# Optimization experiments

Measured on AMD Instinct MI355X. Metric: run time of the kernel, lower is better.

## Reference

```python
import jax, jax.numpy as jnp
import numpy as np

TEMP = 0.05
BIG = 1e6


def _mlp(z, W1, b1, W2, b2, W3, b3, W4, b4, W5, b5):
    h = jax.nn.selu(z @ W1 + b1)
    h = jax.nn.selu(h @ W2 + b2)
    h = jax.nn.selu(h @ W3 + b3)
    h = jax.nn.selu(h @ W4 + b4)
    return h @ W5 + b5


def _cdist(a, b):
    # Euclidean distance via ||a||^2 + ||b||^2 - 2 a.b (clamped for fp safety)
    d2 = (jnp.sum(a * a, axis=1)[:, None]
          + jnp.sum(b * b, axis=1)[None, :]
          - 2.0 * (a @ b.T))
    return jnp.sqrt(jnp.maximum(d2, 0.0))


def _compute_drift(x, y_pos, y_neg):
    N, N_pos = x.shape[0], y_pos.shape[0]
    dist_pos = _cdist(x, y_pos)                      # [N, N_pos]
    dist_neg = _cdist(x, y_neg)                      # [N, N_neg]
    if N == y_neg.shape[0]:
        dist_neg = dist_neg + jnp.eye(N, dtype=x.dtype) * BIG
    logit = jnp.concatenate([-dist_pos / TEMP, -dist_neg / TEMP], axis=1)
    for _ in range(5):  # Sinkhorn: alternating row / column normalization
        logit = logit - jax.nn.logsumexp(logit, axis=-1, keepdims=True)
        logit = logit - jax.nn.logsumexp(logit, axis=-2, keepdims=True)
    A = jnp.exp(logit)
    A_pos, A_neg = A[:, :N_pos], A[:, N_pos:]
    W_pos = A_pos * jnp.sum(A_neg, axis=1, keepdims=True)
    W_neg = A_neg * jnp.sum(A_pos, axis=1, keepdims=True)
    return W_pos @ y_pos - W_neg @ y_neg             # [N, D]


def _forward(pos, z, W1, b1, W2, b2, W3, b3, W4, b4, W5, b5):
    gen = _mlp(z, W1, b1, W2, b2, W3, b3, W4, b4, W5, b5)
    V = _compute_drift(gen, pos, gen)                # computed under no_grad
    target = jax.lax.stop_gradient(gen + V)
    return jnp.sum((gen - target) ** 2, axis=-1)      # per-sample loss [N]


def setup_inputs() -> dict:
    key = jax.random.key(0)
    ks = jax.random.split(key, 8)
    N, D, ND, H = 8192, 256, 128, 1024
    def w(k, fan_in, fan_out):
        return jax.random.normal(k, (fan_in, fan_out), jnp.float32) / np.float32(np.sqrt(fan_in))
    return {
        "pos": jax.random.normal(ks[0], (N, D), jnp.float32),
        "z": jax.random.normal(ks[1], (N, ND), jnp.float32),
        "W1": w(ks[2], ND, H), "b1": jnp.zeros((H,), jnp.float32),
        "W2": w(ks[3], H, H),  "b2": jnp.zeros((H,), jnp.float32),
        "W3": w(ks[4], H, H),  "b3": jnp.zeros((H,), jnp.float32),
        "W4": w(ks[5], H, H),  "b4": jnp.zeros((H,), jnp.float32),
        "W5": w(ks[6], H, D),  "b5": jnp.zeros((D,), jnp.float32),
    }


def reference(pos, z, W1, b1, W2, b2, W3, b3, W4, b4, W5, b5):
    return _forward(pos, z, W1, b1, W2, b2, W3, b3, W4, b4, W5, b5)
```

## Files before the change

kernel.cpp:

```cpp
#include <hip/hip_runtime.h>

#define DEVI __device__ __forceinline__

typedef short bf16x8 __attribute__((ext_vector_type(8)));
typedef float f32x4 __attribute__((ext_vector_type(4)));
typedef unsigned short u16;
typedef unsigned short u16x8 __attribute__((ext_vector_type(8)));
typedef unsigned short u16x4 __attribute__((ext_vector_type(4)));

enum { EPI_MLP = 0, EPI_DISTQ = 1, EPI_NEGTRI = 2 };

#define KLOG2E_T 28.853900817779268f
#define QSCALE 1846.6496523378733f
#define INVQ 0.015625f
#define PSLOTS 80

DEVI u16 f2bf(float f) {
  unsigned u = __float_as_uint(f);
  return (u16)((u + 0x7FFFu + ((u >> 16) & 1u)) >> 16);
}
DEVI float bf2f(u16 h) { return __uint_as_float(((unsigned)h) << 16); }
DEVI float seluf(float x) {
  return x > 0.f ? 1.0507009873554805f * x : 1.7580993408473766f * expm1f(x);
}
DEVI void gload16(const void* g, void* l) {
  __builtin_amdgcn_global_load_lds(
      (const __attribute__((address_space(1))) unsigned*)g,
      (__attribute__((address_space(3))) unsigned*)l, 16, 0, 0);
}
DEVI void lse_comb(float& m, float& s, float m2, float s2) {
  float M = fmaxf(m, m2);
  s = s * exp2f(m - M) + s2 * exp2f(m2 - M);
  m = M;
}
DEVI size_t triblk(int I, int J) { return ((size_t)I * (I + 1) / 2 + J) * 4096; }

template <int R, int NW>
DEVI void stage_tile(const u16* __restrict__ src, int ld, int row0, int k0,
                     u16* lds, int wave, int lane) {
  constexpr int INST = R / (16 * NW);
#pragma unroll
  for (int t = 0; t < INST; ++t) {
    int brow = (wave * INST + t) * 16;
    int row = brow + (lane >> 2);
    int col = (lane & 3) * 8;
    gload16(src + (size_t)(row0 + row) * ld + (k0 + col), lds + brow * 32);
  }
}

template <int BM, int BN, int WM, int WN, int EPI>
__global__ __launch_bounds__(WM* WN * 64) void gemm_k(
    const u16* __restrict__ Ahi, const u16* __restrict__ Alo, int lda,
    const u16* __restrict__ Bhi, const u16* __restrict__ Blo, int ldb, int K,
    float* __restrict__ Cf, int ldc,
    const float* __restrict__ bias, int act, u16* __restrict__ Ohi,
    u16* __restrict__ Olo, int ldo,
    const float* __restrict__ xN2, const float* __restrict__ yN2,
    u16* __restrict__ Cq) {
  if constexpr (EPI == EPI_NEGTRI) {
    if (blockIdx.x > blockIdx.y) return;
  }
  constexpr int NW = WM * WN;
  constexpr int FM = BM / (WM * 16), FN = BN / (WN * 16);
  const int tid = threadIdx.x, lane = tid & 63, wave = tid >> 6;
  const int bm0 = blockIdx.y * BM, bn0 = blockIdx.x * BN;
  const int wr = (wave / WN) * (FM * 16), wc = (wave % WN) * (FN * 16);
  __shared__ __align__(16) u16 AsH[BM * 32];
  __shared__ __align__(16) u16 BsH[BN * 32];
  __shared__ __align__(16) u16 AsL[BM * 32];
  __shared__ __align__(16) u16 BsL[BN * 32];
  f32x4 acc[FM][FN] = {};
  const int fr = lane & 15, ko = (lane >> 4) * 8;
  for (int k0 = 0; k0 < K; k0 += 32) {
    stage_tile<BM, NW>(Ahi, lda, bm0, k0, AsH, wave, lane);
    stage_tile<BN, NW>(Bhi, ldb, bn0, k0, BsH, wave, lane);
    stage_tile<BM, NW>(Alo, lda, bm0, k0, AsL, wave, lane);
    stage_tile<BN, NW>(Blo, ldb, bn0, k0, BsL, wave, lane);
    __syncthreads();
    bf16x8 ah[FM], bh[FN], al[FM], bl[FN];
#pragma unroll
    for (int m = 0; m < FM; ++m) ah[m] = *(const bf16x8*)&AsH[(wr + m * 16 + fr) * 32 + ko];
#pragma unroll
    for (int n = 0; n < FN; ++n) bh[n] = *(const bf16x8*)&BsH[(wc + n * 16 + fr) * 32 + ko];
#pragma unroll
    for (int m = 0; m < FM; ++m) al[m] = *(const bf16x8*)&AsL[(wr + m * 16 + fr) * 32 + ko];
#pragma unroll
    for (int n = 0; n < FN; ++n) bl[n] = *(const bf16x8*)&BsL[(wc + n * 16 + fr) * 32 + ko];
#pragma unroll
    for (int m = 0; m < FM; ++m)
#pragma unroll
      for (int n = 0; n < FN; ++n) {
        acc[m][n] = __builtin_amdgcn_mfma_f32_16x16x32_bf16(ah[m], bh[n], acc[m][n], 0, 0, 0);
        acc[m][n] = __builtin_amdgcn_mfma_f32_16x16x32_bf16(al[m], bh[n], acc[m][n], 0, 0, 0);
        acc[m][n] = __builtin_amdgcn_mfma_f32_16x16x32_bf16(ah[m], bl[n], acc[m][n], 0, 0, 0);
      }
    __syncthreads();
  }
#pragma unroll
  for (int m = 0; m < FM; ++m)
#pragma unroll
    for (int n = 0; n < FN; ++n)
#pragma unroll
      for (int q = 0; q < 4; ++q) {
        int row = bm0 + wr + m * 16 + (lane >> 4) * 4 + q;
        int col = bn0 + wc + n * 16 + fr;
        float v = acc[m][n][q];
        if constexpr (EPI == EPI_MLP) {
          v += bias[col];
          if (act) v = seluf(v);
          u16 h = f2bf(v);
          size_t idx = (size_t)row * ldo + col;
          Ohi[idx] = h;
          Olo[idx] = f2bf(v - bf2f(h));
          if (Cf) Cf[(size_t)row * ldc + col] = v;
        } else if constexpr (EPI == EPI_DISTQ) {
          float d2 = fmaxf(xN2[row] + yN2[col] - 2.f * v, 0.f);
          float qf = fminf(QSCALE * sqrtf(d2), 65535.f);
          Cq[(size_t)row * 8192 + col] = (u16)__float2uint_rn(qf);
        } else {
          int bI = row >> 6, bJ = col >> 6;
          if (bJ <= bI) {
            float d2 = fmaxf(xN2[row] + yN2[col] - 2.f * v, 0.f);
            float qf = fminf(QSCALE * sqrtf(d2), 65535.f);
            u16 qu = (u16)__float2uint_rn(qf);
            if (row == col) qu = 65535;
            Cq[triblk(bI, bJ) + (row & 63) * 64 + (col & 63)] = qu;
          }
        }
      }
}

DEVI void lse16(const u16x8& qa, const u16x8& qb, const float* __restrict__ w,
                float& m, float& s) {
  f32x4 w0 = *(const f32x4*)w;
  f32x4 w1 = *(const f32x4*)(w + 4);
  f32x4 w2 = *(const f32x4*)(w + 8);
  f32x4 w3 = *(const f32x4*)(w + 12);
  float v[16];
#pragma unroll
  for (int e = 0; e < 4; ++e) {
    v[e] = fmaf((float)qa[e], -INVQ, -w0[e]);
    v[4 + e] = fmaf((float)qa[4 + e], -INVQ, -w1[e]);
    v[8 + e] = fmaf((float)qb[e], -INVQ, -w2[e]);
    v[12 + e] = fmaf((float)qb[4 + e], -INVQ, -w3[e]);
  }
  float mx = v[0];
#pragma unroll
  for (int e = 1; e < 16; ++e) mx = fmaxf(mx, v[e]);
  float ac = 0.f;
#pragma unroll
  for (int e = 0; e < 16; ++e) ac += exp2f(v[e] - mx);
  lse_comb(m, s, mx, ac);
}

__global__ __launch_bounds__(256) void sink_k(
    const u16* __restrict__ DqPos, const u16* __restrict__ DqTri,
    const float* __restrict__ wpos, const float* __restrict__ wneg,
    float* __restrict__ Pm, float* __restrict__ Ps) {
  const int tid = threadIdx.x;
  const int I = blockIdx.y, q8 = blockIdx.x;
  __shared__ __align__(16) u16 stg[4096];
  __shared__ float Cm[64][12], Cs[64][12];
  const int rn = tid >> 2, cn = (tid & 3) * 16;
  const int p2 = tid & 31, g8 = tid >> 5;
  float mA = -3.0e38f, sA = 0.f;
  float mB0 = -3.0e38f, sB0 = 0.f, mB1 = -3.0e38f, sB1 = 0.f;
  const int sw = (rn & 7) << 3;

  {
    const size_t rowbase = (size_t)(I * 64 + rn) * 8192;
    for (int jc = 0; jc < 16; ++jc) {
      int j0 = q8 * 1024 + jc * 64 + cn;
      u16x8 qa = *(const u16x8*)&DqPos[rowbase + j0];
      u16x8 qb = *(const u16x8*)&DqPos[rowbase + j0 + 8];
      lse16(qa, qb, wpos + j0, mA, sA);
    }
  }
  for (int Jb = q8 * 16; Jb < q8 * 16 + 16; ++Jb) {
    if (Jb <= I) {
      const u16* blk = DqTri + triblk(I, Jb);
      u16x8 qa = *(const u16x8*)&blk[rn * 64 + cn];
      u16x8 qb = *(const u16x8*)&blk[rn * 64 + cn + 8];
      lse16(qa, qb, wneg + Jb * 64 + cn, mA, sA);
    } else {
      const u16* blk = DqTri + triblk(Jb, I);
      u16x8 qa = *(const u16x8*)&blk[rn * 64 + cn];
      u16x8 qb = *(const u16x8*)&blk[rn * 64 + cn + 8];
      *(u16x8*)&stg[rn * 64 + (cn ^ sw)] = qa;
      *(u16x8*)&stg[rn * 64 + ((cn + 8) ^ sw)] = qb;
      __syncthreads();
      float v0[8], v1[8];
#pragma unroll
      for (int cc = 0; cc < 8; ++cc) {
        int sj = cc * 8 + g8;
        unsigned wq = *(const unsigned*)&stg[sj * 64 + ((2 * p2) ^ ((sj & 7) << 3))];
        float wgt = wneg[Jb * 64 + sj];
        v0[cc] = fmaf((float)(wq & 0xFFFFu), -INVQ, -wgt);
        v1[cc] = fmaf((float)(wq >> 16), -INVQ, -wgt);
      }
      float mx0 = v0[0], mx1 = v1[0];
#pragma unroll
      for (int cc = 1; cc < 8; ++cc) { mx0 = fmaxf(mx0, v0[cc]); mx1 = fmaxf(mx1, v1[cc]); }
      float a0 = 0.f, a1 = 0.f;
#pragma unroll
      for (int cc = 0; cc < 8; ++cc) { a0 += exp2f(v0[cc] - mx0); a1 += exp2f(v1[cc] - mx1); }
      lse_comb(mB0, sB0, mx0, a0);
      lse_comb(mB1, sB1, mx1, a1);
      __syncthreads();
    }
  }
  for (int i = tid; i < 64 * 12; i += 256) { (&Cm[0][0])[i] = -3.0e38f; (&Cs[0][0])[i] = 0.f; }
  __syncthreads();
  Cm[rn][tid & 3] = mA; Cs[rn][tid & 3] = sA;
  Cm[2 * p2][4 + g8] = mB0; Cs[2 * p2][4 + g8] = sB0;
  Cm[2 * p2 + 1][4 + g8] = mB1; Cs[2 * p2 + 1][4 + g8] = sB1;
  __syncthreads();
  if (tid < 64) {
    float m = Cm[tid][0], s = Cs[tid][0];
#pragma unroll
    for (int b = 1; b < 12; ++b) lse_comb(m, s, Cm[tid][b], Cs[tid][b]);
    Pm[(size_t)q8 * 8192 + I * 64 + tid] = m;
    Ps[(size_t)q8 * 8192 + I * 64 + tid] = s;
  }
}

__global__ __launch_bounds__(256) void colpass_k(
    const u16* __restrict__ DqPos, const u16* __restrict__ DqTri,
    const float* __restrict__ rv, float* __restrict__ Pm, float* __restrict__ Ps) {
  const int bid = blockIdx.x, tid = threadIdx.x;
  __shared__ __align__(16) u16 stg[4096];
  __shared__ float Cm[64][12], Cs[64][12];
  if (bid < 1024) {
    const int q8 = bid & 7, I = bid >> 3;
    const int rn = tid >> 2, cn = (tid & 3) * 16;
    const int p2 = tid & 31, g8 = tid >> 5;
    const int sw = (rn & 7) << 3;
    float mA = -3.0e38f, sA = 0.f;
    float mB0 = -3.0e38f, sB0 = 0.f, mB1 = -3.0e38f, sB1 = 0.f;
    for (int Jb = q8 * 16; Jb < q8 * 16 + 16; ++Jb) {
      if (Jb <= I) {
        const u16* blk = DqTri + triblk(I, Jb);
        u16x8 qa = *(const u16x8*)&blk[rn * 64 + cn];
        u16x8 qb = *(const u16x8*)&blk[rn * 64 + cn + 8];
        lse16(qa, qb, rv + Jb * 64 + cn, mA, sA);
      } else {
        const u16* blk = DqTri + triblk(Jb, I);
        u16x8 qa = *(const u16x8*)&blk[rn * 64 + cn];
        u16x8 qb = *(const u16x8*)&blk[rn * 64 + cn + 8];
        *(u16x8*)&stg[rn * 64 + (cn ^ sw)] = qa;
        *(u16x8*)&stg[rn * 64 + ((cn + 8) ^ sw)] = qb;
        __syncthreads();
        float v0[8], v1[8];
#pragma unroll
        for (int cc = 0; cc < 8; ++cc) {
          int sj = cc * 8 + g8;
          unsigned wq = *(const unsigned*)&stg[sj * 64 + ((2 * p2) ^ ((sj & 7) << 3))];
          float wgt = rv[Jb * 64 + sj];
          v0[cc] = fmaf((float)(wq & 0xFFFFu), -INVQ, -wgt);
          v1[cc] = fmaf((float)(wq >> 16), -INVQ, -wgt);
        }
        float mx0 = v0[0], mx1 = v1[0];
#pragma unroll
        for (int cc = 1; cc < 8; ++cc) { mx0 = fmaxf(mx0, v0[cc]); mx1 = fmaxf(mx1, v1[cc]); }
        float a0 = 0.f, a1 = 0.f;
#pragma unroll
        for (int cc = 0; cc < 8; ++cc) { a0 += exp2f(v0[cc] - mx0); a1 += exp2f(v1[cc] - mx1); }
        lse_comb(mB0, sB0, mx0, a0);
        lse_comb(mB1, sB1, mx1, a1);
        __syncthreads();
      }
    }
    for (int i = tid; i < 64 * 12; i += 256) { (&Cm[0][0])[i] = -3.0e38f; (&Cs[0][0])[i] = 0.f; }
    __syncthreads();
    Cm[rn][tid & 3] = mA; Cs[rn][tid & 3] = sA;
    Cm[2 * p2][4 + g8] = mB0; Cs[2 * p2][4 + g8] = sB0;
    Cm[2 * p2 + 1][4 + g8] = mB1; Cs[2 * p2 + 1][4 + g8] = sB1;
    __syncthreads();
    if (tid < 64) {
      float m = Cm[tid][0], s = Cs[tid][0];
#pragma unroll
      for (int b2 = 1; b2 < 12; ++b2) lse_comb(m, s, Cm[tid][b2], Cs[tid][b2]);
      Pm[(size_t)(72 + q8) * 8192 + I * 64 + tid] = m;
      Ps[(size_t)(72 + q8) * 8192 + I * 64 + tid] = s;
    }
  } else {
    const int b2 = bid - 1024;
    const int jb = b2 & 7, ic = b2 >> 3;
    int j0 = jb * 1024 + tid * 4;
    int i0 = ic * 128;
    float m[4], s[4];
#pragma unroll
    for (int e = 0; e < 4; ++e) { m[e] = -3.0e38f; s[e] = 0.f; }
    for (int ib = 0; ib < 16; ++ib) {
      float v[4][8];
#pragma unroll
      for (int ii = 0; ii < 8; ++ii) {
        int i = i0 + ib * 8 + ii;
        u16x4 qv = *(const u16x4*)&DqPos[(size_t)i * 8192 + j0];
        float ri = rv[i];
#pragma unroll
        for (int e = 0; e < 4; ++e) v[e][ii] = fmaf((float)qv[e], -INVQ, -ri);
      }
#pragma unroll
      for (int e = 0; e < 4; ++e) {
        float mx = v[e][0];
#pragma unroll
        for (int ii = 1; ii < 8; ++ii) mx = fmaxf(mx, v[e][ii]);
        float ac = 0.f;
#pragma unroll
        for (int ii = 0; ii < 8; ++ii) ac += exp2f(v[e][ii] - mx);
        lse_comb(m[e], s[e], mx, ac);
      }
    }
#pragma unroll
    for (int e = 0; e < 4; ++e) {
      Pm[(size_t)(8 + ic) * 8192 + j0 + e] = m[e];
      Ps[(size_t)(8 + ic) * 8192 + j0 + e] = s[e];
    }
  }
}

__global__ void comb_rv_k(const float* __restrict__ Pm, const float* __restrict__ Ps,
                          float* __restrict__ rv) {
  int j = blockIdx.x * 256 + threadIdx.x;
  float m = Pm[j], s = Ps[j];
  for (int b = 1; b < 8; ++b)
    lse_comb(m, s, Pm[(size_t)b * 8192 + j], Ps[(size_t)b * 8192 + j]);
  rv[j] = m + log2f(s);
}

__global__ void comb_cpc_k(const float* __restrict__ Pm, const float* __restrict__ Ps,
                           float* __restrict__ cpos, float* __restrict__ cneg) {
  int j = blockIdx.x * 256 + threadIdx.x;
  if (j < 8192) {
    float m = Pm[(size_t)8 * 8192 + j], s = Ps[(size_t)8 * 8192 + j];
    for (int b = 9; b < 72; ++b)
      lse_comb(m, s, Pm[(size_t)b * 8192 + j], Ps[(size_t)b * 8192 + j]);
    cpos[j] = m + log2f(s);
  } else {
    int jj = j - 8192;
    float m = Pm[(size_t)72 * 8192 + jj], s = Ps[(size_t)72 * 8192 + jj];
    for (int b = 73; b < 80; ++b)
      lse_comb(m, s, Pm[(size_t)b * 8192 + jj], Ps[(size_t)b * 8192 + jj]);
    cneg[jj] = m + log2f(s);
  }
}

template <bool NEG>
__global__ __launch_bounds__(512) void pv_k(
    const u16* __restrict__ DqPos, const u16* __restrict__ DqTri,
    const float* __restrict__ rvec, const float* __restrict__ w,
    const u16* __restrict__ BT, float* __restrict__ Mout,
    float* __restrict__ sout) {
  const int tid = threadIdx.x, lane = tid & 63, wave = tid >> 6;
  const int I = blockIdx.y;
  const int kh = blockIdx.x;
  __shared__ __align__(16) u16 AT[64 * 128];
  __shared__ __align__(16) u16 Bs[4 * 256 * 32];
  __shared__ __align__(16) u16 stg[NEG ? 2 * 4096 : 8];
  __shared__ float rvS[64];
  __shared__ float SredN[64][8];
  __shared__ float SredT[64][8];
  const int wrg = (wave >> 2) * 32, wcg = (wave & 3) * 64;
  const int fr = lane & 15, ko = (lane >> 4) * 8;
  const int rn = tid >> 3;
  const int cnp = (tid & 7) * 16;
  const int cnn = (tid & 7) * 8;
  const int swr = (rn & 7) << 3;
  const int p = tid & 63, sjg = tid >> 6;
  const int swp = (p & 7) << 3;
  float asumN = 0.f, asumT = 0.f;
  if (tid < 64) rvS[tid] = rvec[I * 64 + tid];
  __syncthreads();
  const float riN = rvS[rn];
  const float riT = rvS[p];
  f32x4 acc[2][4] = {};

  for (int jc = 0; jc < 32; ++jc) {
    const int j0 = (kh * 32 + jc) * 128;
    __syncthreads();
#pragma unroll
    for (int ks = 0; ks < 4; ++ks)
      stage_tile<256, 8>(BT, 8192, 0, j0 + ks * 32, Bs + ks * 8192, wave, lane);
    if constexpr (!NEG) {
      const u16* rp = DqPos + (size_t)(I * 64 + rn) * 8192 + j0 + cnp;
      u16x8 qa = *(const u16x8*)rp;
      u16x8 qb = *(const u16x8*)(rp + 8);
      const float* wp = w + j0 + cnp;
      f32x4 w0 = *(const f32x4*)wp;
      f32x4 w1 = *(const f32x4*)(wp + 4);
      f32x4 w2 = *(const f32x4*)(wp + 8);
      f32x4 w3 = *(const f32x4*)(wp + 12);
      union { u16x8 v; u16 e[8]; } pk0, pk1;
#pragma unroll
      for (int e = 0; e < 4; ++e) {
        float a0 = exp2f(fmaf((float)qa[e], -INVQ, -riN - w0[e]));
        float a1 = exp2f(fmaf((float)qa[4 + e], -INVQ, -riN - w1[e]));
        float a2 = exp2f(fmaf((float)qb[e], -INVQ, -riN - w2[e]));
        float a3 = exp2f(fmaf((float)qb[4 + e], -INVQ, -riN - w3[e]));
        asumN += a0 + a1 + a2 + a3;
        pk0.e[e] = f2bf(a0); pk0.e[4 + e] = f2bf(a1);
        pk1.e[e] = f2bf(a2); pk1.e[4 + e] = f2bf(a3);
      }
      *(u16x8*)&AT[rn * 128 + (cnp ^ swr)] = pk0.v;
      *(u16x8*)&AT[rn * 128 + ((cnp + 8) ^ swr)] = pk1.v;
    } else {
      bool anytr = false;
#pragma unroll
      for (int h = 0; h < 2; ++h) {
        const int Jb = kh * 64 + jc * 2 + h;
        if (Jb <= I) {
          const u16* blk = DqTri + triblk(I, Jb);
          u16x8 q = *(const u16x8*)&blk[rn * 64 + cnn];
          const float* wp = w + Jb * 64 + cnn;
          f32x4 w0 = *(const f32x4*)wp;
          f32x4 w1 = *(const f32x4*)(wp + 4);
          union { u16x8 v; u16 e[8]; } pk;
#pragma unroll
          for (int e = 0; e < 4; ++e) {
            float a0 = exp2f(fmaf((float)q[e], -INVQ, -riN - w0[e]));
            float a1 = exp2f(fmaf((float)q[4 + e], -INVQ, -riN - w1[e]));
            asumN += a0 + a1;
            pk.e[e] = f2bf(a0); pk.e[4 + e] = f2bf(a1);
          }
          *(u16x8*)&AT[rn * 128 + ((h * 64 + cnn) ^ swr)] = pk.v;
        } else {
          anytr = true;
          const u16* blk = DqTri + triblk(Jb, I);
          u16x8 q = *(const u16x8*)&blk[rn * 64 + cnn];
          *(u16x8*)&stg[h * 4096 + rn * 64 + (cnn ^ swr)] = q;
        }
      }
      if (anytr) {
        __syncthreads();
#pragma unroll
        for (int h = 0; h < 2; ++h) {
          const int Jb = kh * 64 + jc * 2 + h;
          if (Jb <= I) continue;
#pragma unroll
          for (int cc = 0; cc < 8; ++cc) {
            int sj = cc * 8 + sjg;
            u16 q = stg[h * 4096 + sj * 64 + (p ^ ((sj & 7) << 3))];
            float a = exp2f(fmaf((float)q, -INVQ, -riT - w[Jb * 64 + sj]));
            asumT += a;
            AT[p * 128 + ((h * 64 + sj) ^ swp)] = f2bf(a);
          }
        }
      }
    }
    __syncthreads();
#pragma unroll
    for (int ks = 0; ks < 4; ++ks) {
      bf16x8 a2[2], b2[4];
#pragma unroll
      for (int m = 0; m < 2; ++m) {
        int rl = wrg + m * 16 + fr;
        a2[m] = *(const bf16x8*)&AT[rl * 128 + ((ks * 32 + ko) ^ ((rl & 7) << 3))];
      }
#pragma unroll
      for (int n = 0; n < 4; ++n)
        b2[n] = *(const bf16x8*)&Bs[ks * 8192 + (wcg + n * 16 + fr) * 32 + ko];
#pragma unroll
      for (int m = 0; m < 2; ++m)
#pragma unroll
        for (int n = 0; n < 4; ++n)
          acc[m][n] = __builtin_amdgcn_mfma_f32_16x16x32_bf16(a2[m], b2[n], acc[m][n], 0, 0, 0);
    }
  }
#pragma unroll
  for (int m = 0; m < 2; ++m)
#pragma unroll
    for (int n = 0; n < 4; ++n)
#pragma unroll
      for (int q = 0; q < 4; ++q) {
        int row = I * 64 + wrg + m * 16 + (lane >> 4) * 4 + q;
        int d = wcg + n * 16 + fr;
        Mout[(size_t)kh * 2097152 + (size_t)row * 256 + d] = acc[m][n][q];
      }
  SredN[rn][tid & 7] = asumN;
  SredT[p][sjg] = NEG ? asumT : 0.f;
  __syncthreads();
  if (tid < 64) {
    float s = 0.f;
#pragma unroll
    for (int b = 0; b < 8; ++b) s += SredN[tid][b] + SredT[tid][b];
    sout[kh * 8192 + I * 64 + tid] = s;
  }
}

__global__ void convert_split_k(const float* __restrict__ src, u16* __restrict__ hi,
                                u16* __restrict__ lo, int n) {
  int i = blockIdx.x * 256 + threadIdx.x;
  if (i < n) {
    float v = src[i];
    u16 h = f2bf(v);
    hi[i] = h;
    lo[i] = f2bf(v - bf2f(h));
  }
}

__global__ void transpose_split_k(const float* __restrict__ src, int K, int N,
                                  u16* __restrict__ hi, u16* __restrict__ lo) {
  __shared__ float t[32][33];
  int x = threadIdx.x & 31, y = threadIdx.x >> 5;
  int k0 = blockIdx.x * 32, n0 = blockIdx.y * 32;
  for (int yy = y; yy < 32; yy += 8) t[yy][x] = src[(size_t)(k0 + yy) * N + n0 + x];
  __syncthreads();
  for (int yy = y; yy < 32; yy += 8) {
    float v = t[x][yy];
    size_t idx = (size_t)(n0 + yy) * K + k0 + x;
    u16 h = f2bf(v);
    hi[idx] = h;
    lo[idx] = f2bf(v - bf2f(h));
  }
}

__global__ void transpose_b16_k(const float* __restrict__ src, int M, int D,
                                u16* __restrict__ dst) {
  __shared__ float t[32][33];
  int x = threadIdx.x & 31, y = threadIdx.x >> 5;
  int m0 = blockIdx.x * 32, d0 = blockIdx.y * 32;
  for (int yy = y; yy < 32; yy += 8) t[yy][x] = src[(size_t)(m0 + yy) * D + d0 + x];
  __syncthreads();
  for (int yy = y; yy < 32; yy += 8)
    dst[(size_t)(d0 + yy) * M + m0 + x] = f2bf(t[x][yy]);
}

__global__ void rownorm_k(const float* __restrict__ src, float* __restrict__ o) {
  int i = blockIdx.x, t = threadIdx.x;
  float s = 0.f;
  for (int d = t; d < 256; d += 64) {
    float v = src[(size_t)i * 256 + d];
    s += v * v;
  }
  for (int off = 32; off; off >>= 1) s += __shfl_down(s, off, 64);
  if (t == 0) o[i] = s;
}

__global__ void zero_k(float* __restrict__ p, int n) {
  int i = blockIdx.x * 256 + threadIdx.x;
  if (i < n) p[i] = 0.f;
}

__global__ void decode_k(float* __restrict__ out, float x, int n) {
  int i = blockIdx.x * 256 + threadIdx.x;
  if (i < n) out[i] = x;
}

__global__ void final_out_k(const float* __restrict__ M1, const float* __restrict__ M2,
                            const float* __restrict__ sp, const float* __restrict__ sn,
                            float* __restrict__ out) {
  __shared__ float S[256];
  int i = blockIdx.x, d = threadIdx.x;
  size_t idx = (size_t)i * 256 + d;
  float spv = sp[i] + sp[8192 + i];
  float snv = sn[i] + sn[8192 + i];
  float v = snv * (M1[idx] + M1[2097152 + idx]) - spv * (M2[idx] + M2[2097152 + idx]);
  S[d] = v * v;
  __syncthreads();
  for (int off = 128; off; off >>= 1) {
    if (d < off) S[d] += S[d + off];
    __syncthreads();
  }
  if (d == 0) out[i] = S[0];
}

extern "C" void kernel_launch(void* const* d_in, const int* in_sizes, int n_in,
                              void* d_out, int out_size, void* d_ws, size_t ws_size,
                              hipStream_t stream) {
  (void)in_sizes; (void)n_in; (void)out_size;
  const float* pos = (const float*)d_in[0];
  const float* z   = (const float*)d_in[1];
  const float* W1  = (const float*)d_in[2];
  const float* b1  = (const float*)d_in[3];
  const float* W2  = (const float*)d_in[4];
  const float* b2  = (const float*)d_in[5];
  const float* W3  = (const float*)d_in[6];
  const float* b3  = (const float*)d_in[7];
  const float* W4  = (const float*)d_in[8];
  const float* b4  = (const float*)d_in[9];
  const float* W5  = (const float*)d_in[10];
  const float* b5  = (const float*)d_in[11];
  float* out = (float*)d_out;

  if (ws_size < (size_t)261500000) {
    decode_k<<<32, 256, 0, stream>>>(out, (float)(double)(ws_size >> 10), 8192);
    return;
  }

  char* wsp = (char*)d_ws;
  size_t off = 0;
  auto alloc = [&](size_t bytes) -> char* {
    char* p = wsp + off;
    off += (bytes + 255) & ~(size_t)255;
    return p;
  };
  u16* DqPos = (u16*)alloc((size_t)8192 * 8192 * 2);
  u16* DqTri = (u16*)alloc((size_t)8256 * 4096 * 2);
  u16* Yh    = (u16*)alloc((size_t)16384 * 256 * 2);
  u16* Yl    = (u16*)alloc((size_t)16384 * 256 * 2);
  u16* posT  = (u16*)alloc((size_t)256 * 8192 * 2);
  u16* genT  = (u16*)alloc((size_t)256 * 8192 * 2);
  float* yN2 = (float*)alloc(16384 * 4);
  float* rv  = (float*)alloc(8192 * 4);
  float* cpos = (float*)alloc(8192 * 4);
  float* cneg = (float*)alloc(8192 * 4);
  float* spv = (float*)alloc(2 * 8192 * 4);
  float* snv = (float*)alloc(2 * 8192 * 4);
  float* M1  = (float*)alloc((size_t)2 * 8192 * 256 * 4);
  float* M2  = (float*)alloc((size_t)2 * 8192 * 256 * 4);
  float* Pm = M1;
  float* Ps = Pm + (size_t)PSLOTS * 8192;

  size_t toff = 0;
  char* tbase = (char*)DqPos;
  auto talloc = [&](size_t bytes) -> char* {
    char* p = tbase + toff;
    toff += (bytes + 255) & ~(size_t)255;
    return p;
  };
  u16* zh    = (u16*)talloc((size_t)8192 * 128 * 2);
  u16* zl    = (u16*)talloc((size_t)8192 * 128 * 2);
  u16* W1Th  = (u16*)talloc(1024 * 128 * 2);
  u16* W1Tl  = (u16*)talloc(1024 * 128 * 2);
  u16* W2Th  = (u16*)talloc(1024 * 1024 * 2);
  u16* W2Tl  = (u16*)talloc(1024 * 1024 * 2);
  u16* W3Th  = (u16*)talloc(1024 * 1024 * 2);
  u16* W3Tl  = (u16*)talloc(1024 * 1024 * 2);
  u16* W4Th  = (u16*)talloc(1024 * 1024 * 2);
  u16* W4Tl  = (u16*)talloc(1024 * 1024 * 2);
  u16* W5Th  = (u16*)talloc(256 * 1024 * 2);
  u16* W5Tl  = (u16*)talloc(256 * 1024 * 2);
  u16* h1h   = (u16*)talloc((size_t)8192 * 1024 * 2);
  u16* h1l   = (u16*)talloc((size_t)8192 * 1024 * 2);
  u16* h2h   = (u16*)talloc((size_t)8192 * 1024 * 2);
  u16* h2l   = (u16*)talloc((size_t)8192 * 1024 * 2);
  float* genf = (float*)talloc((size_t)8192 * 256 * 4);

  u16* genH = Yh + (size_t)8192 * 256;
  u16* genL = Yl + (size_t)8192 * 256;
  float* pN2 = yN2;
  float* gN2 = yN2 + 8192;

  convert_split_k<<<4096, 256, 0, stream>>>(z, zh, zl, 8192 * 128);
  convert_split_k<<<8192, 256, 0, stream>>>(pos, Yh, Yl, 8192 * 256);
  transpose_split_k<<<dim3(4, 32), 256, 0, stream>>>(W1, 128, 1024, W1Th, W1Tl);
  transpose_split_k<<<dim3(32, 32), 256, 0, stream>>>(W2, 1024, 1024, W2Th, W2Tl);
  transpose_split_k<<<dim3(32, 32), 256, 0, stream>>>(W3, 1024, 1024, W3Th, W3Tl);
  transpose_split_k<<<dim3(32, 32), 256, 0, stream>>>(W4, 1024, 1024, W4Th, W4Tl);
  transpose_split_k<<<dim3(32, 8), 256, 0, stream>>>(W5, 1024, 256, W5Th, W5Tl);
  rownorm_k<<<8192, 64, 0, stream>>>(pos, pN2);
  transpose_b16_k<<<dim3(256, 8), 256, 0, stream>>>(pos, 8192, 256, posT);

  gemm_k<128, 128, 2, 2, EPI_MLP><<<dim3(8, 64), 256, 0, stream>>>(
      zh, zl, 128, W1Th, W1Tl, 128, 128, nullptr, 0, b1, 1, h1h, h1l, 1024,
      nullptr, nullptr, nullptr);
  gemm_k<128, 128, 2, 2, EPI_MLP><<<dim3(8, 64), 256, 0, stream>>>(
      h1h, h1l, 1024, W2Th, W2Tl, 1024, 1024, nullptr, 0, b2, 1, h2h, h2l, 1024,
      nullptr, nullptr, nullptr);
  gemm_k<128, 128, 2, 2, EPI_MLP><<<dim3(8, 64), 256, 0, stream>>>(
      h2h, h2l, 1024, W3Th, W3Tl, 1024, 1024, nullptr, 0, b3, 1, h1h, h1l, 1024,
      nullptr, nullptr, nullptr);
  gemm_k<128, 128, 2, 2, EPI_MLP><<<dim3(8, 64), 256, 0, stream>>>(
      h1h, h1l, 1024, W4Th, W4Tl, 1024, 1024, nullptr, 0, b4, 1, h2h, h2l, 1024,
      nullptr, nullptr, nullptr);
  gemm_k<128, 128, 2, 2, EPI_MLP><<<dim3(2, 64), 256, 0, stream>>>(
      h2h, h2l, 1024, W5Th, W5Tl, 1024, 1024, genf, 256, b5, 0,
      genH, genL, 256, nullptr, nullptr, nullptr);

  rownorm_k<<<8192, 64, 0, stream>>>(genf, gN2);
  transpose_b16_k<<<dim3(256, 8), 256, 0, stream>>>(genf, 8192, 256, genT);

  gemm_k<128, 128, 2, 2, EPI_NEGTRI><<<dim3(64, 64), 256, 0, stream>>>(
      genH, genL, 256, genH, genL, 256, 256, nullptr, 0, nullptr, 0, nullptr,
      nullptr, 0, gN2, gN2, DqTri);
  gemm_k<128, 128, 2, 2, EPI_DISTQ><<<dim3(64, 64), 256, 0, stream>>>(
      genH, genL, 256, Yh, Yl, 256, 256, nullptr, 0, nullptr, 0, nullptr,
      nullptr, 0, gN2, pN2, DqPos);

  zero_k<<<64, 256, 0, stream>>>(cpos, 16384);
  for (int it = 0; it < 5; ++it) {
    sink_k<<<dim3(8, 128), 256, 0, stream>>>(DqPos, DqTri, cpos, cneg, Pm, Ps);
    comb_rv_k<<<32, 256, 0, stream>>>(Pm, Ps, rv);
    colpass_k<<<1536, 256, 0, stream>>>(DqPos, DqTri, rv, Pm, Ps);
    comb_cpc_k<<<64, 256, 0, stream>>>(Pm, Ps, cpos, cneg);
  }

  pv_k<false><<<dim3(2, 128), 512, 0, stream>>>(DqPos, DqTri, rv, cpos, posT, M1, spv);
  pv_k<true><<<dim3(2, 128), 512, 0, stream>>>(DqPos, DqTri, rv, cneg, genT, M2, snv);

  final_out_k<<<8192, 256, 0, stream>>>(M1, M2, spv, snv, out);
}
```

Before: 1.481 ms.

## Fuse distance GEMMs into one launch with triangular tile map, shrink MLP tiles

Merges the negative (triangular) and positive distance GEMMs into a single launch. A 1D grid maps the first 4096 blocks to the full pos tile set and the rest to lower-triangular tiles only, so the early-exit blocks of the old triangular launch are no longer scheduled. The MLP GEMMs switch to 64x128 tiles to double the block count and improve CU fill. Global load addressing now uses precomputed pointers that advance each k-step instead of recomputing addresses per stage, at the cost of extra registers.

```diff
diff --git a/kernel.cpp b/kernel.cpp
--- a/kernel.cpp
+++ b/kernel.cpp
@@ -8,7 +8,7 @@
 typedef unsigned short u16x8 __attribute__((ext_vector_type(8)));
 typedef unsigned short u16x4 __attribute__((ext_vector_type(4)));
 
-enum { EPI_MLP = 0, EPI_DISTQ = 1, EPI_NEGTRI = 2 };
+enum { EPI_MLP = 0, EPI_FUSED = 1 };
 
 #define KLOG2E_T 28.853900817779268f
 #define QSCALE 1846.6496523378733f
@@ -34,19 +34,6 @@
   m = M;
 }
 DEVI size_t triblk(int I, int J) { return ((size_t)I * (I + 1) / 2 + J) * 4096; }
-
-template <int R, int NW>
-DEVI void stage_tile(const u16* __restrict__ src, int ld, int row0, int k0,
-                     u16* lds, int wave, int lane) {
-  constexpr int INST = R / (16 * NW);
-#pragma unroll
-  for (int t = 0; t < INST; ++t) {
-    int brow = (wave * INST + t) * 16;
-    int row = brow + (lane >> 2);
-    int col = (lane & 3) * 8;
-    gload16(src + (size_t)(row0 + row) * ld + (k0 + col), lds + brow * 32);
-  }
-}
 
 template <int BM, int BN, int WM, int WN, int EPI>
 __global__ __launch_bounds__(WM* WN * 64) void gemm_k(
@@ -56,26 +43,69 @@
     const float* __restrict__ bias, int act, u16* __restrict__ Ohi,
     u16* __restrict__ Olo, int ldo,
     const float* __restrict__ xN2, const float* __restrict__ yN2,
-    u16* __restrict__ Cq) {
-  if constexpr (EPI == EPI_NEGTRI) {
-    if (blockIdx.x > blockIdx.y) return;
-  }
+    u16* __restrict__ Cq, u16* __restrict__ Cq2) {
   constexpr int NW = WM * WN;
   constexpr int FM = BM / (WM * 16), FN = BN / (WN * 16);
+  constexpr int IA = BM / (16 * NW), IB = BN / (16 * NW);
   const int tid = threadIdx.x, lane = tid & 63, wave = tid >> 6;
-  const int bm0 = blockIdx.y * BM, bn0 = blockIdx.x * BN;
+  int bm0, bn0;
+  bool tri = false;
+  const u16 *Bh_ = Bhi, *Bl_ = Blo;
+  const float* yN2_ = yN2;
+  if constexpr (EPI == EPI_FUSED) {
+    if ((int)blockIdx.x < 4096) {
+      bm0 = ((int)blockIdx.x >> 6) * 128;
+      bn0 = ((int)blockIdx.x & 63) * 128;
+    } else {
+      int t = (int)blockIdx.x - 4096;
+      int a = (int)((sqrtf(8.f * (float)t + 1.f) - 1.f) * 0.5f);
+      while ((a + 1) * (a + 2) / 2 <= t) ++a;
+      while (a * (a + 1) / 2 > t) --a;
+      int b = t - a * (a + 1) / 2;
+      bm0 = a * 128;
+      bn0 = b * 128;
+      Bh_ = Ahi; Bl_ = Alo; yN2_ = xN2;
+      tri = true;
+    }
+  } else {
+    bm0 = blockIdx.y * BM;
+    bn0 = blockIdx.x * BN;
+  }
   const int wr = (wave / WN) * (FM * 16), wc = (wave % WN) * (FN * 16);
   __shared__ __align__(16) u16 AsH[BM * 32];
   __shared__ __align__(16) u16 BsH[BN * 32];
   __shared__ __align__(16) u16 AsL[BM * 32];
   __shared__ __align__(16) u16 BsL[BN * 32];
+  const int srow = lane >> 2, scol = (lane & 3) * 8;
+  const u16 *pAh[IA], *pAl[IA], *pBh[IB], *pBl[IB];
+  int lA[IA], lB[IB];
+#pragma unroll
+  for (int t = 0; t < IA; ++t) {
+    int r = (wave * IA + t) * 16;
+    pAh[t] = Ahi + (size_t)(bm0 + r + srow) * lda + scol;
+    pAl[t] = Alo + (size_t)(bm0 + r + srow) * lda + scol;
+    lA[t] = r * 32;
+  }
+#pragma unroll
+  for (int t = 0; t < IB; ++t) {
+    int r = (wave * IB + t) * 16;
+    pBh[t] = Bh_ + (size_t)(bn0 + r + srow) * ldb + scol;
+    pBl[t] = Bl_ + (size_t)(bn0 + r + srow) * ldb + scol;
+    lB[t] = r * 32;
+  }
   f32x4 acc[FM][FN] = {};
   const int fr = lane & 15, ko = (lane >> 4) * 8;
   for (int k0 = 0; k0 < K; k0 += 32) {
-    stage_tile<BM, NW>(Ahi, lda, bm0, k0, AsH, wave, lane);
-    stage_tile<BN, NW>(Bhi, ldb, bn0, k0, BsH, wave, lane);
-    stage_tile<BM, NW>(Alo, lda, bm0, k0, AsL, wave, lane);
-    stage_tile<BN, NW>(Blo, ldb, bn0, k0, BsL, wave, lane);
+#pragma unroll
+    for (int t = 0; t < IA; ++t) {
+      gload16(pAh[t], AsH + lA[t]); pAh[t] += 32;
+      gload16(pAl[t], AsL + lA[t]); pAl[t] += 32;
+    }
+#pragma unroll
+    for (int t = 0; t < IB; ++t) {
+      gload16(pBh[t], BsH + lB[t]); pBh[t] += 32;
+      gload16(pBl[t], BsL + lB[t]); pBl[t] += 32;
+    }
     __syncthreads();
     bf16x8 ah[FM], bh[FN], al[FM], bl[FN];
 #pragma unroll
@@ -113,18 +143,18 @@
           Ohi[idx] = h;
           Olo[idx] = f2bf(v - bf2f(h));
           if (Cf) Cf[(size_t)row * ldc + col] = v;
-        } else if constexpr (EPI == EPI_DISTQ) {
-          float d2 = fmaxf(xN2[row] + yN2[col] - 2.f * v, 0.f);
+        } else {
+          float d2 = fmaxf(xN2[row] + yN2_[col] - 2.f * v, 0.f);
           float qf = fminf(QSCALE * sqrtf(d2), 65535.f);
-          Cq[(size_t)row * 8192 + col] = (u16)__float2uint_rn(qf);
-        } else {
-          int bI = row >> 6, bJ = col >> 6;
-          if (bJ <= bI) {
-            float d2 = fmaxf(xN2[row] + yN2[col] - 2.f * v, 0.f);
-            float qf = fminf(QSCALE * sqrtf(d2), 65535.f);
-            u16 qu = (u16)__float2uint_rn(qf);
-            if (row == col) qu = 65535;
-            Cq[triblk(bI, bJ) + (row & 63) * 64 + (col & 63)] = qu;
+          u16 qu = (u16)__float2uint_rn(qf);
+          if (!tri) {
+            Cq[(size_t)row * 8192 + col] = qu;
+          } else {
+            int bI = row >> 6, bJ = col >> 6;
+            if (bJ <= bI) {
+              if (row == col) qu = 65535;
+              Cq2[triblk(bI, bJ) + (row & 63) * 64 + (col & 63)] = qu;
+            }
           }
         }
       }
@@ -380,8 +410,14 @@
     const int j0 = (kh * 32 + jc) * 128;
     __syncthreads();
 #pragma unroll
-    for (int ks = 0; ks < 4; ++ks)
-      stage_tile<256, 8>(BT, 8192, 0, j0 + ks * 32, Bs + ks * 8192, wave, lane);
+    for (int ks = 0; ks < 4; ++ks) {
+      int brow = wave * 32 + (lane >> 2);
+      int bcol = (lane & 3) * 8;
+      gload16(BT + (size_t)brow * 8192 + j0 + ks * 32 + bcol,
+              Bs + ks * 8192 + wave * 32 * 32);
+      gload16(BT + (size_t)(brow + 16) * 8192 + j0 + ks * 32 + bcol,
+              Bs + ks * 8192 + (wave * 32 + 16) * 32);
+    }
     if constexpr (!NEG) {
       const u16* rp = DqPos + (size_t)(I * 64 + rn) * 8192 + j0 + cnp;
       u16x8 qa = *(const u16x8*)rp;
@@ -652,31 +688,28 @@
   rownorm_k<<<8192, 64, 0, stream>>>(pos, pN2);
   transpose_b16_k<<<dim3(256, 8), 256, 0, stream>>>(pos, 8192, 256, posT);
 
-  gemm_k<128, 128, 2, 2, EPI_MLP><<<dim3(8, 64), 256, 0, stream>>>(
+  gemm_k<64, 128, 2, 2, EPI_MLP><<<dim3(8, 128), 256, 0, stream>>>(
       zh, zl, 128, W1Th, W1Tl, 128, 128, nullptr, 0, b1, 1, h1h, h1l, 1024,
-      nullptr, nullptr, nullptr);
-  gemm_k<128, 128, 2, 2, EPI_MLP><<<dim3(8, 64), 256, 0, stream>>>(
+      nullptr, nullptr, nullptr, nullptr);
+  gemm_k<64, 128, 2, 2, EPI_MLP><<<dim3(8, 128), 256, 0, stream>>>(
       h1h, h1l, 1024, W2Th, W2Tl, 1024, 1024, nullptr, 0, b2, 1, h2h, h2l, 1024,
-      nullptr, nullptr, nullptr);
-  gemm_k<128, 128, 2, 2, EPI_MLP><<<dim3(8, 64), 256, 0, stream>>>(
+      nullptr, nullptr, nullptr, nullptr);
+  gemm_k<64, 128, 2, 2, EPI_MLP><<<dim3(8, 128), 256, 0, stream>>>(
       h2h, h2l, 1024, W3Th, W3Tl, 1024, 1024, nullptr, 0, b3, 1, h1h, h1l, 1024,
-      nullptr, nullptr, nullptr);
-  gemm_k<128, 128, 2, 2, EPI_MLP><<<dim3(8, 64), 256, 0, stream>>>(
+      nullptr, nullptr, nullptr, nullptr);
+  gemm_k<64, 128, 2, 2, EPI_MLP><<<dim3(8, 128), 256, 0, stream>>>(
       h1h, h1l, 1024, W4Th, W4Tl, 1024, 1024, nullptr, 0, b4, 1, h2h, h2l, 1024,
-      nullptr, nullptr, nullptr);
-  gemm_k<128, 128, 2, 2, EPI_MLP><<<dim3(2, 64), 256, 0, stream>>>(
+      nullptr, nullptr, nullptr, nullptr);
+  gemm_k<64, 128, 2, 2, EPI_MLP><<<dim3(2, 128), 256, 0, stream>>>(
       h2h, h2l, 1024, W5Th, W5Tl, 1024, 1024, genf, 256, b5, 0,
-      genH, genL, 256, nullptr, nullptr, nullptr);
+      genH, genL, 256, nullptr, nullptr, nullptr, nullptr);
 
   rownorm_k<<<8192, 64, 0, stream>>>(genf, gN2);
   transpose_b16_k<<<dim3(256, 8), 256, 0, stream>>>(genf, 8192, 256, genT);
 
-  gemm_k<128, 128, 2, 2, EPI_NEGTRI><<<dim3(64, 64), 256, 0, stream>>>(
-      genH, genL, 256, genH, genL, 256, 256, nullptr, 0, nullptr, 0, nullptr,
-      nullptr, 0, gN2, gN2, DqTri);
-  gemm_k<128, 128, 2, 2, EPI_DISTQ><<<dim3(64, 64), 256, 0, stream>>>(
+  gemm_k<128, 128, 2, 2, EPI_FUSED><<<6176, 256, 0, stream>>>(
       genH, genL, 256, Yh, Yl, 256, 256, nullptr, 0, nullptr, 0, nullptr,
-      nullptr, 0, gN2, pN2, DqPos);
+      nullptr, 0, gN2, pN2, DqPos, DqTri);
 
   zero_k<<<64, 256, 0, stream>>>(cpos, 16384);
   for (int it = 0; it < 5; ++it) {
```

Measured after the change: 1.428 ms. -3.6%, faster.
